# Kernel tuning notes

Measured on AMD Instinct MI355X. Metric: run time of the kernel, lower is better.

## Reference

```python
import jax, jax.numpy as jnp
import numpy as np

LN_EPS = 1e-5


def _gather(x, idx):
    # x: [B, N, C], idx: [B, N, K] -> [B, N, K, C]
    return jax.vmap(lambda xb, ib: xb[ib])(x, idx)


def setup_inputs() -> dict:
    key = jax.random.key(0)
    ks = jax.random.split(key, 8)
    B, N, K, C_in, C_out, GEO = 2, 16384, 32, 128, 128, 10
    return {
        "points": jax.random.normal(ks[0], (B, N, 3), dtype=jnp.float32),
        "features": jax.random.normal(ks[1], (B, N, C_in), dtype=jnp.float32),
        "grouped_idx": jax.random.randint(ks[2], (B, N, K), 0, N, dtype=jnp.int32),
        "w_pos": jax.random.normal(ks[3], (GEO, C_in), dtype=jnp.float32) * (GEO ** -0.5),
        "b_pos": jnp.zeros((C_in,), jnp.float32),
        "w_gcm": jax.random.normal(ks[4], (C_in, C_in), dtype=jnp.float32) * (C_in ** -0.5),
        "b_gcm": jnp.zeros((C_in,), jnp.float32),
        "w_out": jax.random.normal(ks[5], (C_in, C_out), dtype=jnp.float32) * (C_in ** -0.5),
        "b_out": jnp.zeros((C_out,), jnp.float32),
        "ln_g": jnp.ones((C_out,), jnp.float32),
        "ln_b": jnp.zeros((C_out,), jnp.float32),
    }


def reference(points, features, grouped_idx, w_pos, b_pos, w_gcm, b_gcm,
              w_out, b_out, ln_g, ln_b):
    # gather neighbor coords and features: [B, N, K, *]
    grouped_pts = _gather(points, grouped_idx)
    xyz = points[..., 0:3]                      # [B, N, 3]
    grouped_xyz = grouped_pts[..., 0:3]         # [B, N, K, 3]
    center = xyz[:, :, None, :]                 # [B, N, 1, 3]
    diff = grouped_xyz - center                 # xi - xj
    dist = jnp.linalg.norm(diff, axis=-1, keepdims=True)  # ||xi - xj||
    K = grouped_xyz.shape[2]
    geo = jnp.concatenate(
        [jnp.broadcast_to(center, grouped_xyz.shape), grouped_xyz, diff, dist],
        axis=-1)                                # [B, N, K, 10]
    expanded_f = geo @ w_pos + b_pos            # pos_proj -> [B, N, K, C_in]
    grouped_f = _gather(features, grouped_idx)  # [B, N, K, C_in]
    h = jax.nn.relu((grouped_f + expanded_f) @ w_gcm + b_gcm)  # gcm_layer
    pooled = jnp.max(h, axis=2)                 # maxpooling over neighbors
    res = pooled + features                     # residual
    o = res @ w_out + b_out                     # out Linear
    mu = jnp.mean(o, axis=-1, keepdims=True)
    var = jnp.mean((o - mu) ** 2, axis=-1, keepdims=True)
    o = (o - mu) * jax.lax.rsqrt(var + LN_EPS) * ln_g + ln_b  # LayerNorm
    return jax.nn.relu(o)
```

## Files before the change

kernel.cpp:

```cpp
#include <hip/hip_runtime.h>
#include <hip/hip_bf16.h>
#include <math.h>

typedef __attribute__((ext_vector_type(8))) short short8;
typedef __attribute__((ext_vector_type(4))) short short4v;
typedef __attribute__((ext_vector_type(4))) float float4v;
typedef unsigned short ushort_t;

constexpr int NPTS = 32768;
constexpr int NN   = 16384;
constexpr int KK   = 32;
constexpr int CC   = 128;
constexpr int GRP  = 16;
constexpr int SG   = 40;
constexpr int SR   = 136;
#define LN_EPS 1e-5f

constexpr size_t WS_WP   = 0;
constexpr size_t WS_WO   = 40960;
constexpr size_t WS_BE   = 73728;
constexpr size_t WS_PG   = 74240;
constexpr size_t WS_FB   = 79360;
constexpr size_t WS_NEED = WS_FB + (size_t)NPTS * CC * 2;

__device__ __forceinline__ short f2bs(float x) {
    return (short)__builtin_bit_cast(unsigned short, __float2bfloat16(x));
}
__device__ __forceinline__ float bs2f(ushort_t u) {
    return __uint_as_float(((unsigned)u) << 16);
}

__global__ __launch_bounds__(128) void prep_fold(
    const float* __restrict__ w_pos, const float* __restrict__ b_pos,
    const float* __restrict__ w_gcm, const float* __restrict__ b_gcm,
    float* __restrict__ wsPG, float* __restrict__ wsBeff)
{
    const int c = threadIdx.x, g = blockIdx.x;
    if (g < 10) {
        float s = 0.f;
        #pragma unroll
        for (int r = 0; r < 128; ++r) s += w_pos[g * 128 + r] * w_gcm[r * 128 + c];
        wsPG[g * 128 + c] = s;
    } else {
        float s = b_gcm[c];
        #pragma unroll
        for (int r = 0; r < 128; ++r) s += b_pos[r] * w_gcm[r * 128 + c];
        wsBeff[c] = s;
    }
}

__global__ __launch_bounds__(256) void prep_pack(
    const float* __restrict__ features, const float* __restrict__ w_gcm,
    const float* __restrict__ w_out, const float* __restrict__ wsPG,
    short* __restrict__ wsWp, short* __restrict__ wsWo, ushort_t* __restrict__ featbf,
    int do_convert)
{
    const int t = threadIdx.x, blk = blockIdx.x;
    if (blk < 512) {
        if (!do_convert) return;
        const int base = blk * 2048 + t;
        #pragma unroll
        for (int i = 0; i < 8; ++i) {
            const int f4 = base + i * 256;
            const float4 a = ((const float4*)features)[f4];
            short4v v; v[0]=f2bs(a.x); v[1]=f2bs(a.y); v[2]=f2bs(a.z); v[3]=f2bs(a.w);
            ((short4v*)featbf)[f4] = v;
        }
        return;
    }
    if (blk == 512) {
        #pragma unroll 4
        for (int e = t; e < 16 * 128 * 8; e += 256) {
            const int j = e & 7, n = (e >> 3) & 127, g = e >> 10;
            wsWp[e] = f2bs(w_gcm[(g * 8 + j) * 128 + n]);
        }
        return;
    }
    if (blk == 513) {
        #pragma unroll 4
        for (int e2 = t; e2 < 4 * 128 * 8; e2 += 256) {
            const int e = 16 * 128 * 8 + e2;
            const int j = e & 7, n = (e >> 3) & 127, g = e >> 10;
            const int k = g * 8 + j;
            wsWp[e] = (k < 138) ? f2bs(wsPG[(k - 128) * 128 + n]) : (short)0;
        }
        return;
    }
    #pragma unroll 4
    for (int e = t; e < 128 * 128; e += 256) {
        const int j = e & 7, n = (e >> 3) & 127, g = e >> 10;
        wsWo[e] = f2bs(w_out[(g * 8 + j) * 128 + n]);
    }
}

template<int DMA>
__global__ __launch_bounds__(256) void bridge_main(
    const float* __restrict__ points, const float* __restrict__ features,
    const int*   __restrict__ gidx,
    const short* __restrict__ wsWp, const short* __restrict__ wsWo,
    const float* __restrict__ wsBeff, const ushort_t* __restrict__ featbf,
    const float* __restrict__ b_out, const float* __restrict__ ln_g,
    const float* __restrict__ ln_b,
    float* __restrict__ out)
{
    __shared__ short sA[2][KK * CC];
    __shared__ short sG[2][KK * SG];
    __shared__ short sRes[GRP * SR];
    __shared__ int   sIdx[GRP * KK];
    __shared__ float sPS[4][GRP], sPQ[4][GRP];

    const int t = threadIdx.x, wv = t >> 6, lane = t & 63;
    const int quad = (t >> 4) & 3, m = t & 15;
    const int g0 = blockIdx.x * GRP;
    const int nbase = (g0 >= NN) ? NN : 0;
    const int col0 = wv * 32 + m;

    sIdx[t]       = gidx[(size_t)g0 * KK + t];
    sIdx[t + 256] = gidx[(size_t)g0 * KK + t + 256];
    if (t < 128) {
        const int b = t >> 6, r = (t >> 1) & 31, h = t & 1;
        *(short8*)&sG[b][r * SG + 16 + h * 8] = (short8)0;
    }

    short8 bWp[5][2];
    #pragma unroll
    for (int ks = 0; ks < 5; ++ks)
        #pragma unroll
        for (int ntl = 0; ntl < 2; ++ntl)
            bWp[ks][ntl] = *((const short8*)wsWp + ((ks * 4 + quad) * 128 + col0 + ntl * 16));
    float beffv[2] = { wsBeff[col0], wsBeff[col0 + 16] };

    __syncthreads();

    const int r0 = wv * 4 + (lane >> 4);
    const int pc = lane & 15;
    const int gc = pc ^ r0;

    float4 ff0a, ff0b, ff1a, ff1b;
    float gcx, gcy, gcz, ggx, ggy, ggz;

    auto issue_dma = [&](int p, int buf) {
        const int kn0 = nbase + sIdx[p * KK + r0];
        const int kn1 = nbase + sIdx[p * KK + r0 + 16];
        const ushort_t* gp0 = featbf + (size_t)kn0 * CC + gc * 8;
        const ushort_t* gp1 = featbf + (size_t)kn1 * CC + gc * 8;
        short* l0 = &sA[buf][(wv * 4) * CC];
        short* l1 = &sA[buf][(wv * 4 + 16) * CC];
        __builtin_amdgcn_global_load_lds((const __attribute__((address_space(1))) void*)gp0,
                                         (__attribute__((address_space(3))) void*)l0, 16, 0, 0);
        __builtin_amdgcn_global_load_lds((const __attribute__((address_space(1))) void*)gp1,
                                         (__attribute__((address_space(3))) void*)l1, 16, 0, 0);
    };
    auto fb_load = [&](int p) {
        const int kn0 = nbase + sIdx[p * KK + r0];
        const int kn1 = nbase + sIdx[p * KK + r0 + 16];
        const float4* f0 = (const float4*)(features + (size_t)kn0 * CC + gc * 8);
        const float4* f1 = (const float4*)(features + (size_t)kn1 * CC + gc * 8);
        ff0a = f0[0]; ff0b = f0[1]; ff1a = f1[0]; ff1b = f1[1];
    };
    auto fb_store = [&](int buf) {
        short8 v;
        v[0]=f2bs(ff0a.x); v[1]=f2bs(ff0a.y); v[2]=f2bs(ff0a.z); v[3]=f2bs(ff0a.w);
        v[4]=f2bs(ff0b.x); v[5]=f2bs(ff0b.y); v[6]=f2bs(ff0b.z); v[7]=f2bs(ff0b.w);
        *(short8*)&sA[buf][r0 * CC + pc * 8] = v;
        v[0]=f2bs(ff1a.x); v[1]=f2bs(ff1a.y); v[2]=f2bs(ff1a.z); v[3]=f2bs(ff1a.w);
        v[4]=f2bs(ff1b.x); v[5]=f2bs(ff1b.y); v[6]=f2bs(ff1b.z); v[7]=f2bs(ff1b.w);
        *(short8*)&sA[buf][(r0 + 16) * CC + pc * 8] = v;
    };
    auto geo_load = [&](int p) {
        if (lane < 8) {
            const int j  = wv * 8 + lane;
            const int pt = g0 + p;
            const int kn = nbase + sIdx[p * KK + j];
            gcx = points[(size_t)pt * 3 + 0]; gcy = points[(size_t)pt * 3 + 1]; gcz = points[(size_t)pt * 3 + 2];
            ggx = points[(size_t)kn * 3 + 0]; ggy = points[(size_t)kn * 3 + 1]; ggz = points[(size_t)kn * 3 + 2];
        }
    };
    auto geo_store = [&](int buf) {
        if (lane < 8) {
            const int j = wv * 8 + lane;
            const float dx = ggx - gcx, dy = ggy - gcy, dz = ggz - gcz;
            const float dist = sqrtf(dx * dx + dy * dy + dz * dz);
            short8 v0, v1 = (short8)0;
            v0[0]=f2bs(gcx); v0[1]=f2bs(gcy); v0[2]=f2bs(gcz);
            v0[3]=f2bs(ggx); v0[4]=f2bs(ggy); v0[5]=f2bs(ggz);
            v0[6]=f2bs(dx);  v0[7]=f2bs(dy);
            v1[0]=f2bs(dz);  v1[1]=f2bs(dist);
            *(short8*)&sG[buf][j * SG + 0] = v0;
            *(short8*)&sG[buf][j * SG + 8] = v1;
        }
    };

    if constexpr (DMA) issue_dma(0, 0); else fb_load(0);
    geo_load(0);
    if constexpr (!DMA) fb_store(0);
    geo_store(0);
    __syncthreads();

    int offA[4];
    #pragma unroll
    for (int ks = 0; ks < 4; ++ks) offA[ks] = m * CC + (((ks * 4 + quad) ^ m) * 8);
    const int offG = m * SG + quad * 8;

    for (int p = 0; p < GRP; ++p) {
        const int buf = p & 1, nbuf = buf ^ 1;
        if (p + 1 < GRP) {
            if constexpr (DMA) issue_dma(p + 1, nbuf); else fb_load(p + 1);
            geo_load(p + 1);
        }

        const short* ab = sA[buf];
        const short* ag = sG[buf];
        float4v acc[2][2] = {};
        #pragma unroll
        for (int ks = 0; ks < 4; ++ks) {
            const short8 a0 = *(const short8*)(ab + offA[ks]);
            const short8 a1 = *(const short8*)(ab + offA[ks] + 16 * CC);
            acc[0][0] = __builtin_amdgcn_mfma_f32_16x16x32_bf16(a0, bWp[ks][0], acc[0][0], 0, 0, 0);
            acc[0][1] = __builtin_amdgcn_mfma_f32_16x16x32_bf16(a0, bWp[ks][1], acc[0][1], 0, 0, 0);
            acc[1][0] = __builtin_amdgcn_mfma_f32_16x16x32_bf16(a1, bWp[ks][0], acc[1][0], 0, 0, 0);
            acc[1][1] = __builtin_amdgcn_mfma_f32_16x16x32_bf16(a1, bWp[ks][1], acc[1][1], 0, 0, 0);
        }
        {
            const short8 a0 = *(const short8*)(ag + offG);
            const short8 a1 = *(const short8*)(ag + offG + 16 * SG);
            acc[0][0] = __builtin_amdgcn_mfma_f32_16x16x32_bf16(a0, bWp[4][0], acc[0][0], 0, 0, 0);
            acc[0][1] = __builtin_amdgcn_mfma_f32_16x16x32_bf16(a0, bWp[4][1], acc[0][1], 0, 0, 0);
            acc[1][0] = __builtin_amdgcn_mfma_f32_16x16x32_bf16(a1, bWp[4][0], acc[1][0], 0, 0, 0);
            acc[1][1] = __builtin_amdgcn_mfma_f32_16x16x32_bf16(a1, bWp[4][1], acc[1][1], 0, 0, 0);
        }

        if (p + 1 < GRP) {
            if constexpr (!DMA) fb_store(nbuf);
            geo_store(nbuf);
        }

        const int pt = g0 + p;
        #pragma unroll
        for (int ntl = 0; ntl < 2; ++ntl) {
            float v = acc[0][ntl][0];
            #pragma unroll
            for (int r = 1; r < 4; ++r) v = fmaxf(v, acc[0][ntl][r]);
            #pragma unroll
            for (int r = 0; r < 4; ++r) v = fmaxf(v, acc[1][ntl][r]);
            v = fmaxf(v, __shfl_xor(v, 16));
            v = fmaxf(v, __shfl_xor(v, 32));
            v = fmaxf(v + beffv[ntl], 0.f);
            float fc;
            if constexpr (DMA) fc = bs2f(featbf[(size_t)pt * CC + col0 + ntl * 16]);
            else               fc = features[(size_t)pt * CC + col0 + ntl * 16];
            const float res = v + fc;
            if (quad == 0) sRes[p * SR + col0 + ntl * 16] = f2bs(res);
        }
        __syncthreads();
    }

    short8 bWo[4][2];
    #pragma unroll
    for (int ks = 0; ks < 4; ++ks)
        #pragma unroll
        for (int ntl = 0; ntl < 2; ++ntl)
            bWo[ks][ntl] = *((const short8*)wsWo + ((ks * 4 + quad) * 128 + col0 + ntl * 16));

    const short* rm = sRes + m * SR;
    float4v acc2[2] = {};
    #pragma unroll
    for (int ks = 0; ks < 4; ++ks) {
        const short8 a = *(const short8*)(rm + ks * 32 + quad * 8);
        acc2[0] = __builtin_amdgcn_mfma_f32_16x16x32_bf16(a, bWo[ks][0], acc2[0], 0, 0, 0);
        acc2[1] = __builtin_amdgcn_mfma_f32_16x16x32_bf16(a, bWo[ks][1], acc2[1], 0, 0, 0);
    }

    const float boutv[2] = { b_out[col0], b_out[col0 + 16] };
    const float lngv[2]  = { ln_g[col0], ln_g[col0 + 16] };
    const float lnbv[2]  = { ln_b[col0], ln_b[col0 + 16] };

    #pragma unroll
    for (int r = 0; r < 4; ++r) {
        const float o0 = acc2[0][r] + boutv[0];
        const float o1 = acc2[1][r] + boutv[1];
        float ss = o0 + o1, qq = o0 * o0 + o1 * o1;
        #pragma unroll
        for (int d = 1; d < 16; d <<= 1) { ss += __shfl_xor(ss, d); qq += __shfl_xor(qq, d); }
        if (m == 0) { sPS[wv][quad * 4 + r] = ss; sPQ[wv][quad * 4 + r] = qq; }
    }
    __syncthreads();

    #pragma unroll
    for (int r = 0; r < 4; ++r) {
        const int R = quad * 4 + r;
        const float S = sPS[0][R] + sPS[1][R] + sPS[2][R] + sPS[3][R];
        const float Q = sPQ[0][R] + sPQ[1][R] + sPQ[2][R] + sPQ[3][R];
        const float mu  = S * (1.f / 128.f);
        const float var = fmaxf(Q * (1.f / 128.f) - mu * mu, 0.f);
        const float rstd = rsqrtf(var + LN_EPS);
        const float o0 = acc2[0][r] + boutv[0];
        const float o1 = acc2[1][r] + boutv[1];
        const size_t base = (size_t)(g0 + R) * CC;
        out[base + col0]      = fmaxf((o0 - mu) * rstd * lngv[0] + lnbv[0], 0.f);
        out[base + col0 + 16] = fmaxf((o1 - mu) * rstd * lngv[1] + lnbv[1], 0.f);
    }
}

extern "C" void kernel_launch(void* const* d_in, const int* in_sizes, int n_in,
                              void* d_out, int out_size, void* d_ws, size_t ws_size,
                              hipStream_t stream) {
    const float* points   = (const float*)d_in[0];
    const float* features = (const float*)d_in[1];
    const int*   gidx     = (const int*)  d_in[2];
    const float* w_pos    = (const float*)d_in[3];
    const float* b_pos    = (const float*)d_in[4];
    const float* w_gcm    = (const float*)d_in[5];
    const float* b_gcm    = (const float*)d_in[6];
    const float* w_out    = (const float*)d_in[7];
    const float* b_out    = (const float*)d_in[8];
    const float* ln_g     = (const float*)d_in[9];
    const float* ln_b     = (const float*)d_in[10];
    float* out = (float*)d_out;

    char* ws = (char*)d_ws;
    short*    wsWp   = (short*)(ws + WS_WP);
    short*    wsWo   = (short*)(ws + WS_WO);
    float*    wsBeff = (float*)(ws + WS_BE);
    float*    wsPG   = (float*)(ws + WS_PG);
    ushort_t* featbf = (ushort_t*)(ws + WS_FB);

    const bool use_dma = (ws_size >= WS_NEED);

    hipLaunchKernelGGL(prep_fold, dim3(11), dim3(128), 0, stream,
                       w_pos, b_pos, w_gcm, b_gcm, wsPG, wsBeff);
    hipLaunchKernelGGL(prep_pack, dim3(515), dim3(256), 0, stream,
                       features, w_gcm, w_out, wsPG, wsWp, wsWo, featbf,
                       use_dma ? 1 : 0);
    if (use_dma) {
        hipLaunchKernelGGL((bridge_main<1>), dim3(NPTS / GRP), dim3(256), 0, stream,
                           points, features, gidx, wsWp, wsWo, wsBeff, featbf,
                           b_out, ln_g, ln_b, out);
    } else {
        hipLaunchKernelGGL((bridge_main<0>), dim3(NPTS / GRP), dim3(256), 0, stream,
                           points, features, gidx, wsWp, wsWo, wsBeff, featbf,
                           b_out, ln_g, ln_b, out);
    }
}
```

Measured before the change: 162.7 us.

## Merge prep kernels and shrink main kernel LDS footprint for higher occupancy

Folds the weight-fold prep kernel into the pack kernel, so one launch is removed and the folded position weights live in shared memory. In the main kernel the neighbour indices are stored as 16-bit values, the residual row pitch shrinks, and the LayerNorm partial sums reuse the geometry buffer. Launch bounds now request 6 blocks per CU. Together these reduce LDS and register pressure to raise occupancy, at the cost of possible register spills and LDS bank conflicts from the new pitch.

```diff
diff --git a/kernel.cpp b/kernel.cpp
--- a/kernel.cpp
+++ b/kernel.cpp
@@ -13,13 +13,12 @@
 constexpr int CC   = 128;
 constexpr int GRP  = 16;
 constexpr int SG   = 40;
-constexpr int SR   = 136;
+constexpr int SR   = 132;
 #define LN_EPS 1e-5f
 
 constexpr size_t WS_WP   = 0;
 constexpr size_t WS_WO   = 40960;
 constexpr size_t WS_BE   = 73728;
-constexpr size_t WS_PG   = 74240;
 constexpr size_t WS_FB   = 79360;
 constexpr size_t WS_NEED = WS_FB + (size_t)NPTS * CC * 2;
 
@@ -30,32 +29,17 @@
     return __uint_as_float(((unsigned)u) << 16);
 }
 
-__global__ __launch_bounds__(128) void prep_fold(
+__global__ __launch_bounds__(256) void prep_all(
+    const float* __restrict__ features,
     const float* __restrict__ w_pos, const float* __restrict__ b_pos,
     const float* __restrict__ w_gcm, const float* __restrict__ b_gcm,
-    float* __restrict__ wsPG, float* __restrict__ wsBeff)
+    const float* __restrict__ w_out,
+    short* __restrict__ wsWp, short* __restrict__ wsWo, float* __restrict__ wsBeff,
+    ushort_t* __restrict__ featbf, int do_convert)
 {
-    const int c = threadIdx.x, g = blockIdx.x;
-    if (g < 10) {
-        float s = 0.f;
-        #pragma unroll
-        for (int r = 0; r < 128; ++r) s += w_pos[g * 128 + r] * w_gcm[r * 128 + c];
-        wsPG[g * 128 + c] = s;
-    } else {
-        float s = b_gcm[c];
-        #pragma unroll
-        for (int r = 0; r < 128; ++r) s += b_pos[r] * w_gcm[r * 128 + c];
-        wsBeff[c] = s;
-    }
-}
-
-__global__ __launch_bounds__(256) void prep_pack(
-    const float* __restrict__ features, const float* __restrict__ w_gcm,
-    const float* __restrict__ w_out, const float* __restrict__ wsPG,
-    short* __restrict__ wsWp, short* __restrict__ wsWo, ushort_t* __restrict__ featbf,
-    int do_convert)
-{
+    __shared__ float sPG[10 * 128];
     const int t = threadIdx.x, blk = blockIdx.x;
+
     if (blk < 512) {
         if (!do_convert) return;
         const int base = blk * 2048 + t;
@@ -77,12 +61,27 @@
         return;
     }
     if (blk == 513) {
+        const int c = t & 127, half = t >> 7;
+        for (int gi = 0; gi < 5; ++gi) {
+            const int g = gi * 2 + half;
+            float s = 0.f;
+            #pragma unroll
+            for (int r = 0; r < 128; ++r) s += w_pos[g * 128 + r] * w_gcm[r * 128 + c];
+            sPG[g * 128 + c] = s;
+        }
+        if (t < 128) {
+            float s = b_gcm[t];
+            #pragma unroll
+            for (int r = 0; r < 128; ++r) s += b_pos[r] * w_gcm[r * 128 + t];
+            wsBeff[t] = s;
+        }
+        __syncthreads();
         #pragma unroll 4
         for (int e2 = t; e2 < 4 * 128 * 8; e2 += 256) {
             const int e = 16 * 128 * 8 + e2;
             const int j = e & 7, n = (e >> 3) & 127, g = e >> 10;
             const int k = g * 8 + j;
-            wsWp[e] = (k < 138) ? f2bs(wsPG[(k - 128) * 128 + n]) : (short)0;
+            wsWp[e] = (k < 138) ? f2bs(sPG[(k - 128) * 128 + n]) : (short)0;
         }
         return;
     }
@@ -94,7 +93,7 @@
 }
 
 template<int DMA>
-__global__ __launch_bounds__(256) void bridge_main(
+__global__ __launch_bounds__(256, 6) void bridge_main(
     const float* __restrict__ points, const float* __restrict__ features,
     const int*   __restrict__ gidx,
     const short* __restrict__ wsWp, const short* __restrict__ wsWo,
@@ -106,8 +105,10 @@
     __shared__ short sA[2][KK * CC];
     __shared__ short sG[2][KK * SG];
     __shared__ short sRes[GRP * SR];
-    __shared__ int   sIdx[GRP * KK];
-    __shared__ float sPS[4][GRP], sPQ[4][GRP];
+    __shared__ ushort_t sIdx[GRP * KK];
+
+    float* sPS = (float*)&sG[0][0];
+    float* sPQ = sPS + 4 * GRP;
 
     const int t = threadIdx.x, wv = t >> 6, lane = t & 63;
     const int quad = (t >> 4) & 3, m = t & 15;
@@ -115,8 +116,8 @@
     const int nbase = (g0 >= NN) ? NN : 0;
     const int col0 = wv * 32 + m;
 
-    sIdx[t]       = gidx[(size_t)g0 * KK + t];
-    sIdx[t + 256] = gidx[(size_t)g0 * KK + t + 256];
+    sIdx[t]       = (ushort_t)gidx[(size_t)g0 * KK + t];
+    sIdx[t + 256] = (ushort_t)gidx[(size_t)g0 * KK + t + 256];
     if (t < 128) {
         const int b = t >> 6, r = (t >> 1) & 31, h = t & 1;
         *(short8*)&sG[b][r * SG + 16 + h * 8] = (short8)0;
@@ -282,15 +283,15 @@
         float ss = o0 + o1, qq = o0 * o0 + o1 * o1;
         #pragma unroll
         for (int d = 1; d < 16; d <<= 1) { ss += __shfl_xor(ss, d); qq += __shfl_xor(qq, d); }
-        if (m == 0) { sPS[wv][quad * 4 + r] = ss; sPQ[wv][quad * 4 + r] = qq; }
+        if (m == 0) { sPS[wv * GRP + quad * 4 + r] = ss; sPQ[wv * GRP + quad * 4 + r] = qq; }
     }
     __syncthreads();
 
     #pragma unroll
     for (int r = 0; r < 4; ++r) {
         const int R = quad * 4 + r;
-        const float S = sPS[0][R] + sPS[1][R] + sPS[2][R] + sPS[3][R];
-        const float Q = sPQ[0][R] + sPQ[1][R] + sPQ[2][R] + sPQ[3][R];
+        const float S = sPS[0 * GRP + R] + sPS[1 * GRP + R] + sPS[2 * GRP + R] + sPS[3 * GRP + R];
+        const float Q = sPQ[0 * GRP + R] + sPQ[1 * GRP + R] + sPQ[2 * GRP + R] + sPQ[3 * GRP + R];
         const float mu  = S * (1.f / 128.f);
         const float var = fmaxf(Q * (1.f / 128.f) - mu * mu, 0.f);
         const float rstd = rsqrtf(var + LN_EPS);
@@ -322,16 +323,13 @@
     short*    wsWp   = (short*)(ws + WS_WP);
     short*    wsWo   = (short*)(ws + WS_WO);
     float*    wsBeff = (float*)(ws + WS_BE);
-    float*    wsPG   = (float*)(ws + WS_PG);
     ushort_t* featbf = (ushort_t*)(ws + WS_FB);
 
     const bool use_dma = (ws_size >= WS_NEED);
 
-    hipLaunchKernelGGL(prep_fold, dim3(11), dim3(128), 0, stream,
-                       w_pos, b_pos, w_gcm, b_gcm, wsPG, wsBeff);
-    hipLaunchKernelGGL(prep_pack, dim3(515), dim3(256), 0, stream,
-                       features, w_gcm, w_out, wsPG, wsWp, wsWo, featbf,
-                       use_dma ? 1 : 0);
+    hipLaunchKernelGGL(prep_all, dim3(515), dim3(256), 0, stream,
+                       features, w_pos, b_pos, w_gcm, b_gcm, w_out,
+                       wsWp, wsWo, wsBeff, featbf, use_dma ? 1 : 0);
     if (use_dma) {
         hipLaunchKernelGGL((bridge_main<1>), dim3(NPTS / GRP), dim3(256), 0, stream,
                            points, features, gidx, wsWp, wsWo, wsBeff, featbf,
```

Result: slower. 233.3 us (+43.4%).
